# Kernel tuning notes

Measured on AMD Instinct MI355X. Metric: run time of the kernel, lower is better.

Reference implementation:

```python
import jax, jax.numpy as jnp
import numpy as np

FEATURE_SIZE = 128  # H = W = feature_size per __init__
BATCH = 8


def setup_inputs() -> dict:
    key = jax.random.key(0)
    # uniform [0,1): threshold >0.5 marks ~half the pixels as 'boundary'
    feature_map = jax.random.uniform(key, (BATCH, 1, FEATURE_SIZE, FEATURE_SIZE), dtype=jnp.float32)
    return {"feature_map": feature_map}


def reference(feature_map):
    """Distance transform: for each pixel (i,j), min Euclidean distance to any
    boundary pixel (feature_map > 0.5), where the boundary set is pooled over
    batch+channel (matching torch.where on the full tensor) and the resulting
    scalar is broadcast to every batch element (matching output[:, :, i, j] = min).
    """
    B, C, H, W = feature_map.shape
    ch = jnp.arange(H, dtype=feature_map.dtype)
    cw = jnp.arange(W, dtype=feature_map.dtype)
    dx2 = (ch[:, None] - ch[None, :]) ** 2  # [H(h), H(i)]
    dy2 = (cw[:, None] - cw[None, :]) ** 2  # [W(w), W(j)]
    # boundary positions, unioned over batch/channel (grid is batch-independent)
    mask = jnp.any(feature_map > 0.5, axis=(0, 1))  # [H, W]
    # all-pairs squared distances: axes (h, w, i, j)
    d2 = dx2[:, None, :, None] + dy2[None, :, None, :]  # [H, W, H, W]
    masked = jnp.where(mask[:, :, None, None], d2, jnp.inf)
    dist = jnp.sqrt(jnp.min(masked, axis=(0, 1)))  # [H, W]; sqrt(min)=min(sqrt)
    return jnp.broadcast_to(dist[None, None], (B, C, H, W))
```

## Files before the change

kernel.cpp:

```cpp
#include <hip/hip_runtime.h>
#include <math.h>

#define H_DIM 128
#define W_DIM 128
#define BATCH 8
#define NPIX (H_DIM * W_DIM)
#define INF_I (1 << 28)

__global__ __launch_bounds__(256) void mask_kernel(const float* __restrict__ fm,
                                                   unsigned char* __restrict__ mask) {
    const int idx4 = blockIdx.x * 256 + threadIdx.x;
    const float4* fm4 = (const float4*)fm;
    bool m0 = false, m1 = false, m2 = false, m3 = false;
    #pragma unroll
    for (int b = 0; b < BATCH; ++b) {
        float4 v = fm4[b * 4096 + idx4];
        m0 |= v.x > 0.5f;
        m1 |= v.y > 0.5f;
        m2 |= v.z > 0.5f;
        m3 |= v.w > 0.5f;
    }
    uchar4 mm;
    mm.x = (unsigned char)m0;
    mm.y = (unsigned char)m1;
    mm.z = (unsigned char)m2;
    mm.w = (unsigned char)m3;
    ((uchar4*)mask)[idx4] = mm;
}

__global__ __launch_bounds__(256) void dt_kernel(const unsigned char* __restrict__ mask,
                                                 float* __restrict__ out) {
    const int i = blockIdx.x;
    const int tid = threadIdx.x;

    __shared__ unsigned char maskS[NPIX];
    __shared__ int gpart[2][W_DIM];
    __shared__ int gS[W_DIM];
    __shared__ int bpart[2][W_DIM];
    __shared__ float distS[W_DIM];

    const float4* m4 = (const float4*)mask;
    #pragma unroll
    for (int q = 0; q < 4; ++q)
        ((float4*)maskS)[q * 256 + tid] = m4[q * 256 + tid];
    __syncthreads();

    const int w = tid & 127;
    const int half = tid >> 7;

    {
        int g = INF_I;
        const int h0 = half * 64;
        #pragma unroll 4
        for (int hh = 0; hh < 64; ++hh) {
            const int h = h0 + hh;
            const int d = i - h;
            if (maskS[h * W_DIM + w]) g = min(g, d * d);
        }
        gpart[half][w] = g;
    }
    __syncthreads();
    if (tid < W_DIM) gS[tid] = min(gpart[0][tid], gpart[1][tid]);
    __syncthreads();

    {
        const int j = w;
        int best = INF_I;
        const int w0 = half * 64;
        #pragma unroll 4
        for (int ww = 0; ww < 64; ++ww) {
            const int wc = w0 + ww;
            const int d = j - wc;
            best = min(best, gS[wc] + d * d);
        }
        bpart[half][j] = best;
    }
    __syncthreads();
    if (tid < W_DIM) {
        const int best = min(bpart[0][tid], bpart[1][tid]);
        distS[tid] = (best >= INF_I) ? INFINITY : sqrtf((float)best);
    }
    __syncthreads();

    const int j = tid & 127;
    const int bh = tid >> 7;
    const float v = distS[j];
    #pragma unroll
    for (int k = 0; k < 4; ++k) {
        const int b = bh * 4 + k;
        out[b * NPIX + i * W_DIM + j] = v;
    }
}

extern "C" void kernel_launch(void* const* d_in, const int* in_sizes, int n_in,
                              void* d_out, int out_size, void* d_ws, size_t ws_size,
                              hipStream_t stream) {
    const float* fm = (const float*)d_in[0];
    float* out = (float*)d_out;
    unsigned char* mask = (unsigned char*)d_ws;

    mask_kernel<<<16, 256, 0, stream>>>(fm, mask);
    dt_kernel<<<H_DIM, 256, 0, stream>>>(mask, out);
}
```

Measured before the change: 57.94 us.

## Fuse mask reduction into distance-transform kernel with multiple rows per block

Merges the mask-building kernel into the distance-transform kernel, so each block reads the full 8-batch input and builds the boundary mask in shared memory itself, removing one launch and the global mask round trip. Each 512-thread block now handles 4 output rows, giving 32 blocks, and the column and row min reductions are split four ways. In exchange every block re-reads the whole 512KB input (32x redundant reads, mostly from cache), and the grid is small relative to the CU count, so parallelism is lower.

Measured after the change: 63.89 us. 1.1x slower.

```diff
diff --git a/kernel.cpp b/kernel.cpp
--- a/kernel.cpp
+++ b/kernel.cpp
@@ -6,89 +6,90 @@
 #define BATCH 8
 #define NPIX (H_DIM * W_DIM)
 #define INF_I (1 << 28)
+#define ROWS_PER_BLOCK 4
+#define NBLOCKS (H_DIM / ROWS_PER_BLOCK)
+#define NTHREADS 512
 
-__global__ __launch_bounds__(256) void mask_kernel(const float* __restrict__ fm,
-                                                   unsigned char* __restrict__ mask) {
-    const int idx4 = blockIdx.x * 256 + threadIdx.x;
-    const float4* fm4 = (const float4*)fm;
-    bool m0 = false, m1 = false, m2 = false, m3 = false;
-    #pragma unroll
-    for (int b = 0; b < BATCH; ++b) {
-        float4 v = fm4[b * 4096 + idx4];
-        m0 |= v.x > 0.5f;
-        m1 |= v.y > 0.5f;
-        m2 |= v.z > 0.5f;
-        m3 |= v.w > 0.5f;
-    }
-    uchar4 mm;
-    mm.x = (unsigned char)m0;
-    mm.y = (unsigned char)m1;
-    mm.z = (unsigned char)m2;
-    mm.w = (unsigned char)m3;
-    ((uchar4*)mask)[idx4] = mm;
-}
-
-__global__ __launch_bounds__(256) void dt_kernel(const unsigned char* __restrict__ mask,
-                                                 float* __restrict__ out) {
-    const int i = blockIdx.x;
+__global__ __launch_bounds__(NTHREADS) void fused_dt_kernel(
+    const float* __restrict__ fm, float* __restrict__ out) {
     const int tid = threadIdx.x;
 
     __shared__ unsigned char maskS[NPIX];
-    __shared__ int gpart[2][W_DIM];
+    __shared__ int gpart[4][W_DIM];
     __shared__ int gS[W_DIM];
-    __shared__ int bpart[2][W_DIM];
+    __shared__ int bpart[4][W_DIM];
     __shared__ float distS[W_DIM];
 
-    const float4* m4 = (const float4*)mask;
+    const float4* fm4 = (const float4*)fm;
     #pragma unroll
-    for (int q = 0; q < 4; ++q)
-        ((float4*)maskS)[q * 256 + tid] = m4[q * 256 + tid];
+    for (int q = 0; q < 8; ++q) {
+        const int idx4 = q * NTHREADS + tid;
+        bool m0 = false, m1 = false, m2 = false, m3 = false;
+        #pragma unroll
+        for (int b = 0; b < BATCH; ++b) {
+            float4 v = fm4[b * 4096 + idx4];
+            m0 |= v.x > 0.5f;
+            m1 |= v.y > 0.5f;
+            m2 |= v.z > 0.5f;
+            m3 |= v.w > 0.5f;
+        }
+        uchar4 mm;
+        mm.x = (unsigned char)m0;
+        mm.y = (unsigned char)m1;
+        mm.z = (unsigned char)m2;
+        mm.w = (unsigned char)m3;
+        ((uchar4*)maskS)[idx4] = mm;
+    }
     __syncthreads();
 
     const int w = tid & 127;
-    const int half = tid >> 7;
+    const int quarter = tid >> 7;
 
-    {
-        int g = INF_I;
-        const int h0 = half * 64;
-        #pragma unroll 4
-        for (int hh = 0; hh < 64; ++hh) {
-            const int h = h0 + hh;
-            const int d = i - h;
-            if (maskS[h * W_DIM + w]) g = min(g, d * d);
+    for (int r = 0; r < ROWS_PER_BLOCK; ++r) {
+        const int i = blockIdx.x * ROWS_PER_BLOCK + r;
+
+        {
+            int g = INF_I;
+            const int h0 = quarter * 32;
+            #pragma unroll 4
+            for (int hh = 0; hh < 32; ++hh) {
+                const int h = h0 + hh;
+                const int d = i - h;
+                if (maskS[h * W_DIM + w]) g = min(g, d * d);
+            }
+            gpart[quarter][w] = g;
         }
-        gpart[half][w] = g;
-    }
-    __syncthreads();
-    if (tid < W_DIM) gS[tid] = min(gpart[0][tid], gpart[1][tid]);
-    __syncthreads();
+        __syncthreads();
+        if (tid < W_DIM)
+            gS[tid] = min(min(gpart[0][tid], gpart[1][tid]),
+                          min(gpart[2][tid], gpart[3][tid]));
+        __syncthreads();
 
-    {
-        const int j = w;
-        int best = INF_I;
-        const int w0 = half * 64;
-        #pragma unroll 4
-        for (int ww = 0; ww < 64; ++ww) {
-            const int wc = w0 + ww;
-            const int d = j - wc;
-            best = min(best, gS[wc] + d * d);
+        {
+            int best = INF_I;
+            const int w0 = quarter * 32;
+            #pragma unroll 4
+            for (int ww = 0; ww < 32; ++ww) {
+                const int wc = w0 + ww;
+                const int d = w - wc;
+                best = min(best, gS[wc] + d * d);
+            }
+            bpart[quarter][w] = best;
         }
-        bpart[half][j] = best;
-    }
-    __syncthreads();
-    if (tid < W_DIM) {
-        const int best = min(bpart[0][tid], bpart[1][tid]);
-        distS[tid] = (best >= INF_I) ? INFINITY : sqrtf((float)best);
-    }
-    __syncthreads();
+        __syncthreads();
+        if (tid < W_DIM) {
+            const int best = min(min(bpart[0][tid], bpart[1][tid]),
+                                 min(bpart[2][tid], bpart[3][tid]));
+            distS[tid] = (best >= INF_I) ? INFINITY : sqrtf((float)best);
+        }
+        __syncthreads();
 
-    const int j = tid & 127;
-    const int bh = tid >> 7;
-    const float v = distS[j];
-    #pragma unroll
-    for (int k = 0; k < 4; ++k) {
-        const int b = bh * 4 + k;
-        out[b * NPIX + i * W_DIM + j] = v;
+        const float v = distS[w];
+        #pragma unroll
+        for (int k = 0; k < 2; ++k) {
+            const int b = quarter * 2 + k;
+            out[b * NPIX + i * W_DIM + w] = v;
+        }
     }
 }
 
@@ -97,8 +98,5 @@
                               hipStream_t stream) {
     const float* fm = (const float*)d_in[0];
     float* out = (float*)d_out;
-    unsigned char* mask = (unsigned char*)d_ws;
-
-    mask_kernel<<<16, 256, 0, stream>>>(fm, mask);
-    dt_kernel<<<H_DIM, 256, 0, stream>>>(mask, out);
+    fused_dt_kernel<<<NBLOCKS, NTHREADS, 0, stream>>>(fm, out);
 }
```
